# Performance work log

Hardware: AMD Instinct MI355X
Metric: run time of the kernel (lower is better)

## Reference

```python
import jax, jax.numpy as jnp
import numpy as np

D_MODEL, D_K, D_V = 1024, 64, 64
B, S = 4, 4096

def setup_inputs() -> dict:
    key = jax.random.key(0)
    ks = jax.random.split(key, 9)
    s_in = 1.0 / np.sqrt(D_MODEL)
    return {
        "Q": jax.random.normal(ks[0], (B, S, D_MODEL), jnp.float32),
        "K": jax.random.normal(ks[1], (B, S, D_MODEL), jnp.float32),
        "V": jax.random.normal(ks[2], (B, S, D_MODEL), jnp.float32),
        "Wq": jax.random.uniform(ks[3], (D_MODEL, D_K), jnp.float32, -s_in, s_in),
        "bq": jax.random.uniform(ks[4], (D_K,), jnp.float32, -s_in, s_in),
        "Wk": jax.random.uniform(ks[5], (D_MODEL, D_K), jnp.float32, -s_in, s_in),
        "bk": jax.random.uniform(ks[6], (D_K,), jnp.float32, -s_in, s_in),
        "Wv": jax.random.uniform(ks[7], (D_MODEL, D_V), jnp.float32, -s_in, s_in),
        "bv": jax.random.uniform(ks[8], (D_V,), jnp.float32, -s_in, s_in),
    }

def reference(Q, K, V, Wq, bq, Wk, bk, Wv, bv):
    # Linear projections: [B,S,d_model] -> [B,S,d_k/d_v]
    q = jnp.einsum("bsm,mk->bsk", Q, Wq) + bq
    k = jnp.einsum("btm,mk->btk", K, Wk) + bk
    v = jnp.einsum("btm,mv->btv", V, Wv) + bv
    # Scaled dot-product attention, softmax over key axis (dim=2)
    scores = jnp.einsum("bsk,btk->bst", q, k) / jnp.sqrt(jnp.float32(D_K))
    attn = jax.nn.softmax(scores, axis=2)  # [B,S,S]
    return jnp.einsum("bst,btv->bsv", attn, v)
```

## Files before the change

kernel.cpp:

```cpp
#include <hip/hip_runtime.h>

typedef __bf16 bf16;
typedef __attribute__((ext_vector_type(8))) __bf16 bf16x8;
typedef __attribute__((ext_vector_type(4))) float f32x4;
typedef __attribute__((ext_vector_type(16))) float f32x16;

#define MFMA16(a, b, c) __builtin_amdgcn_mfma_f32_16x16x32_bf16((a), (b), (c), 0, 0, 0)
#define MFMA32(a, b, c) __builtin_amdgcn_mfma_f32_32x32x16_bf16((a), (b), (c), 0, 0, 0)

typedef __attribute__((address_space(3))) unsigned int lds_u32_t;
typedef __attribute__((address_space(1))) unsigned int glb_u32_t;

__device__ __forceinline__ void gl2lds16(const void* g, void* l) {
    __builtin_amdgcn_global_load_lds((const glb_u32_t*)g, (lds_u32_t*)l, 16, 0, 0);
}

__device__ __forceinline__ bf16 tobf(float f) {
    unsigned u = __float_as_uint(f);
    u += 0x7fffu + ((u >> 16) & 1u);
    unsigned short h = (unsigned short)(u >> 16);
    bf16 r;
    __builtin_memcpy(&r, &h, 2);
    return r;
}

__device__ __forceinline__ bf16x8 cvt8h(f32x4 a, f32x4 b) {
    bf16x8 r;
    r[0] = (bf16)a[0]; r[1] = (bf16)a[1]; r[2] = (bf16)a[2]; r[3] = (bf16)a[3];
    r[4] = (bf16)b[0]; r[5] = (bf16)b[1]; r[6] = (bf16)b[2]; r[7] = (bf16)b[3];
    return r;
}

__global__ void wconv_kernel(const float* __restrict__ Wq, const float* __restrict__ Wk,
                             const float* __restrict__ Wv, bf16* __restrict__ Wt) {
    int j = blockIdx.y;
    const float* W = (j == 0) ? Wq : ((j == 1) ? Wk : Wv);
    int idx = blockIdx.x * 256 + threadIdx.x;
    int m = idx >> 6, n = idx & 63;
    Wt[(size_t)j * 65536 + (size_t)n * 1024 + m] = tobf(W[idx]);
}

__launch_bounds__(256, 3)
__global__ void proj_kernel(const float* __restrict__ Q, const float* __restrict__ K,
                            const float* __restrict__ V, const bf16* __restrict__ Wt,
                            const float* __restrict__ bq, const float* __restrict__ bk,
                            const float* __restrict__ bv,
                            bf16* __restrict__ q_ws, bf16* __restrict__ k_ws,
                            bf16* __restrict__ vT_ws) {
    const int j = blockIdx.y;
    const float* In   = (j == 0) ? Q : ((j == 1) ? K : V);
    const float* bias = (j == 0) ? bq : ((j == 1) ? bk : bv);
    const bf16* W = Wt + (size_t)j * 65536;

    __shared__ char smem[49152];
    char* As = smem;
    char* Bs = smem + 32768;

    const int tid = threadIdx.x;
    const int wave = tid >> 6, lane = tid & 63;
    const int quad = lane >> 4, l16 = lane & 15;
    const int rbase_blk = blockIdx.x * 64;

    f32x4 acc[4];
#pragma unroll
    for (int nt = 0; nt < 4; nt++) acc[nt] = {0.f, 0.f, 0.f, 0.f};

    for (int kc = 0; kc < 1024; kc += 128) {
#pragma unroll
        for (int i = 0; i < 8; i++) {
            int u = i * 256 + tid;
            int row = u >> 5, cg = u & 31;
            int cgg = cg ^ (row & 31);
            const float* g = In + (size_t)(rbase_blk + row) * 1024 + kc + cgg * 4;
            gl2lds16(g, As + (size_t)(i * 256 + wave * 64) * 16);
        }
#pragma unroll
        for (int i = 0; i < 4; i++) {
            int u = i * 256 + tid;
            int n = u >> 4, cg = u & 15;
            int cgg = cg ^ (n & 15);
            const bf16* g = W + (size_t)n * 1024 + kc + cgg * 8;
            gl2lds16(g, Bs + (size_t)(i * 256 + wave * 64) * 16);
        }
        __syncthreads();

        const int r = wave * 16 + l16;
#pragma unroll
        for (int p = 0; p < 4; p++) {
            int cg0 = (p * 8 + quad * 2) ^ (r & 31);
            int cg1 = (p * 8 + quad * 2 + 1) ^ (r & 31);
            f32x4 a0 = *(const f32x4*)(As + (size_t)r * 512 + cg0 * 16);
            f32x4 a1 = *(const f32x4*)(As + (size_t)r * 512 + cg1 * 16);
            bf16x8 av = cvt8h(a0, a1);
#pragma unroll
            for (int nt = 0; nt < 4; nt++) {
                int n = nt * 16 + l16;
                int cgb = (p * 4 + quad) ^ (n & 15);
                bf16x8 bv = *(const bf16x8*)(Bs + (size_t)n * 256 + cgb * 16);
                acc[nt] = MFMA16(av, bv, acc[nt]);
            }
        }
        __syncthreads();
    }

    const float scale = (j == 0) ? 0.125f * 1.44269504088896f : 1.0f;

    if (j != 2) {
        bf16* dst = (j == 0) ? q_ws : k_ws;
#pragma unroll
        for (int nt = 0; nt < 4; nt++) {
            int n = nt * 16 + l16;
            float bb = bias[n];
#pragma unroll
            for (int r4 = 0; r4 < 4; r4++) {
                int row = rbase_blk + wave * 16 + quad * 4 + r4;
                dst[(size_t)row * 64 + n] = tobf((acc[nt][r4] + bb) * scale);
            }
        }
    } else {
        bf16 (*vtile)[72] = (bf16(*)[72])smem;
#pragma unroll
        for (int nt = 0; nt < 4; nt++) {
            int n = nt * 16 + l16;
            float bb = bias[n];
#pragma unroll
            for (int r4 = 0; r4 < 4; r4++) {
                vtile[n][wave * 16 + quad * 4 + r4] = tobf(acc[nt][r4] + bb);
            }
        }
        __syncthreads();
        int gb = rbase_blk;
        int bi = gb >> 12, t0 = gb & 4095;
        int d = tid >> 2, part = (tid & 3) * 16;
        bf16x8 x0 = *(const bf16x8*)&vtile[d][part];
        bf16x8 x1 = *(const bf16x8*)&vtile[d][part + 8];
        bf16* dst = vT_ws + (size_t)(bi * 64 + d) * 4096 + t0 + part;
        *(bf16x8*)dst = x0;
        *(bf16x8*)(dst + 8) = x1;
    }
}

__launch_bounds__(256, 4)
__global__ void attn_kernel(const bf16* __restrict__ q_ws, const bf16* __restrict__ k_ws,
                            const bf16* __restrict__ vT_ws,
                            float* __restrict__ po, float* __restrict__ pl,
                            float* __restrict__ out, int keys_per_split, int direct) {
    const int b = blockIdx.z, split = blockIdx.y;
    const int tid = threadIdx.x, wave = tid >> 6, lane = tid & 63;
    const int l32 = lane & 31, h = lane >> 5;

    __shared__ bf16 kt[64][72];
    __shared__ bf16 vt[64][72];
    __shared__ bf16 pt[4][32][72];

    const int qrow0 = b * 4096 + blockIdx.x * 128 + wave * 32;

    bf16x8 qf[4];
    const bf16* qp = q_ws + (size_t)(qrow0 + l32) * 64 + h * 8;
#pragma unroll
    for (int c = 0; c < 4; c++) qf[c] = *(const bf16x8*)(qp + c * 16);

    f32x16 o0, o1;
    float l[16];
#pragma unroll
    for (int i = 0; i < 16; i++) { o0[i] = 0.f; o1[i] = 0.f; l[i] = 0.f; }

    const int key0 = split * keys_per_split;
    const int srow = tid >> 3, scol = (tid & 7) * 8;
    const bf16* kg = k_ws + (size_t)(b * 4096 + key0 + srow) * 64 + scol;
    const bf16* vg = vT_ws + (size_t)(b * 64 + srow) * 4096 + key0 + scol;

    uint4 kv0 = *(const uint4*)kg;
    uint4 kv1 = *(const uint4*)(kg + 2048);
    uint4 vv0 = *(const uint4*)vg;
    uint4 vv1 = *(const uint4*)(vg + 131072);

    for (int t0 = 0; t0 < keys_per_split; t0 += 64) {
        __syncthreads();
        *(uint4*)&kt[srow][scol]      = kv0;
        *(uint4*)&kt[srow + 32][scol] = kv1;
        *(uint4*)&vt[srow][scol]      = vv0;
        *(uint4*)&vt[srow + 32][scol] = vv1;
        if (t0 + 64 < keys_per_split) {
            kv0 = *(const uint4*)(kg + (size_t)(t0 + 64) * 64);
            kv1 = *(const uint4*)(kg + (size_t)(t0 + 64) * 64 + 2048);
            vv0 = *(const uint4*)(vg + t0 + 64);
            vv1 = *(const uint4*)(vg + t0 + 64 + 131072);
        }
        __syncthreads();

#pragma unroll
        for (int kt32 = 0; kt32 < 2; kt32++) {
            f32x16 s;
#pragma unroll
            for (int i = 0; i < 16; i++) s[i] = 0.f;
#pragma unroll
            for (int c = 0; c < 4; c++) {
                bf16x8 kf = *(const bf16x8*)(&kt[kt32 * 32 + l32][c * 16 + h * 8]);
                s = MFMA32(qf[c], kf, s);
            }
#pragma unroll
            for (int i = 0; i < 16; i++) {
                float p = __builtin_amdgcn_exp2f(s[i]);
                l[i] += p;
                int R = (i & 3) + 8 * (i >> 2) + 4 * h;
                pt[wave][R][kt32 * 32 + l32] = (bf16)p;
            }
        }

#pragma unroll
        for (int tc = 0; tc < 4; tc++) {
            bf16x8 pf  = *(const bf16x8*)(&pt[wave][l32][tc * 16 + h * 8]);
            bf16x8 vf0 = *(const bf16x8*)(&vt[l32][tc * 16 + h * 8]);
            bf16x8 vf1 = *(const bf16x8*)(&vt[32 + l32][tc * 16 + h * 8]);
            o0 = MFMA32(pf, vf0, o0);
            o1 = MFMA32(pf, vf1, o1);
        }
    }

#pragma unroll
    for (int i = 0; i < 16; i++) {
        float v = l[i];
        v += __shfl_xor(v, 1);  v += __shfl_xor(v, 2);  v += __shfl_xor(v, 4);
        v += __shfl_xor(v, 8);  v += __shfl_xor(v, 16);
        l[i] = v;
    }

    if (direct) {
        float* orow = out + (size_t)qrow0 * 64;
#pragma unroll
        for (int i = 0; i < 16; i++) {
            int R = (i & 3) + 8 * (i >> 2) + 4 * h;
            float inv = 1.0f / l[i];
            orow[(size_t)R * 64 + l32]      = o0[i] * inv;
            orow[(size_t)R * 64 + 32 + l32] = o1[i] * inv;
        }
    } else {
        size_t prow = (size_t)split * 16384 + qrow0;
        float* pob = po + prow * 64;
#pragma unroll
        for (int i = 0; i < 16; i++) {
            int R = (i & 3) + 8 * (i >> 2) + 4 * h;
            pob[(size_t)R * 64 + l32]      = o0[i];
            pob[(size_t)R * 64 + 32 + l32] = o1[i];
            if (l32 == 0) pl[prow + R] = l[i];
        }
    }
}

__launch_bounds__(256)
__global__ void combine_kernel(const float* __restrict__ po, const float* __restrict__ pl,
                               float* __restrict__ out, int nsplit) {
    int idx = blockIdx.x * 256 + threadIdx.x;
    int row = idx >> 6;
    float so = 0.f, sl = 0.f;
    for (int s = 0; s < nsplit; s++) {
        so += po[(size_t)s * 1048576 + idx];
        sl += pl[(size_t)s * 16384 + row];
    }
    out[idx] = so / sl;
}

extern "C" void kernel_launch(void* const* d_in, const int* in_sizes, int n_in,
                              void* d_out, int out_size, void* d_ws, size_t ws_size,
                              hipStream_t stream) {
    const float* Q  = (const float*)d_in[0];
    const float* K  = (const float*)d_in[1];
    const float* V  = (const float*)d_in[2];
    const float* Wq = (const float*)d_in[3];
    const float* bq = (const float*)d_in[4];
    const float* Wk = (const float*)d_in[5];
    const float* bk = (const float*)d_in[6];
    const float* Wv = (const float*)d_in[7];
    const float* bv = (const float*)d_in[8];
    float* out = (float*)d_out;

    char* ws = (char*)d_ws;
    bf16* Wt    = (bf16*)ws;
    bf16* q_ws  = (bf16*)(ws + 393216);
    bf16* k_ws  = (bf16*)(ws + 393216 + 2097152);
    bf16* vT_ws = (bf16*)(ws + 393216 + 2 * 2097152);
    const size_t base = 393216 + 3 * 2097152;

    const size_t per_split = 16384u * 4u + 1048576u * 4u;
    int nsplit = 1;
    if (ws_size >= base + 8 * per_split) nsplit = 8;
    else if (ws_size >= base + 4 * per_split) nsplit = 4;
    else if (ws_size >= base + 2 * per_split) nsplit = 2;

    float* pl = (float*)(ws + base);
    float* po = (float*)(ws + base + (size_t)nsplit * 65536);

    hipLaunchKernelGGL(wconv_kernel, dim3(256, 3), dim3(256), 0, stream, Wq, Wk, Wv, Wt);
    hipLaunchKernelGGL(proj_kernel, dim3(256, 3), dim3(256), 0, stream,
                       Q, K, V, Wt, bq, bk, bv, q_ws, k_ws, vT_ws);
    hipLaunchKernelGGL(attn_kernel, dim3(32, nsplit, 4), dim3(256), 0, stream,
                       q_ws, k_ws, vT_ws, po, pl, out, 4096 / nsplit, nsplit == 1 ? 1 : 0);
    if (nsplit > 1) {
        hipLaunchKernelGGL(combine_kernel, dim3(4096), dim3(256), 0, stream, po, pl, out, nsplit);
    }
}
```

Measured before the change: 260.3 us.

## Swap QK operand order, XOR-swizzle attention LDS tiles, shrink projection blocks

The attention kernel now computes S transposed, with K as the A operand, so each lane holds one query row's scores. This turns the per-row sum into one lane-local accumulator plus a single shuffle, replacing sixteen five-step reductions, and lets P be written to LDS as packed 4-element stores. The K, V and P LDS tiles drop their padding and use an XOR swizzle to avoid bank conflicts. The projection kernel moves to 128-thread blocks covering 32 rows with 64-wide K chunks and smaller LDS, doubling the grid. The row-sum lookup at the end now needs per-row shuffles, and the smaller projection tiles reuse weights less.

```diff
diff --git a/kernel.cpp b/kernel.cpp
--- a/kernel.cpp
+++ b/kernel.cpp
@@ -1,6 +1,7 @@
 #include <hip/hip_runtime.h>
 
 typedef __bf16 bf16;
+typedef __attribute__((ext_vector_type(4))) __bf16 bf16x4;
 typedef __attribute__((ext_vector_type(8))) __bf16 bf16x8;
 typedef __attribute__((ext_vector_type(4))) float f32x4;
 typedef __attribute__((ext_vector_type(16))) float f32x16;
@@ -40,7 +41,7 @@
     Wt[(size_t)j * 65536 + (size_t)n * 1024 + m] = tobf(W[idx]);
 }
 
-__launch_bounds__(256, 3)
+__launch_bounds__(128, 3)
 __global__ void proj_kernel(const float* __restrict__ Q, const float* __restrict__ K,
                             const float* __restrict__ V, const bf16* __restrict__ Wt,
                             const float* __restrict__ bq, const float* __restrict__ bk,
@@ -52,51 +53,51 @@
     const float* bias = (j == 0) ? bq : ((j == 1) ? bk : bv);
     const bf16* W = Wt + (size_t)j * 65536;
 
-    __shared__ char smem[49152];
+    __shared__ char smem[16384];
     char* As = smem;
-    char* Bs = smem + 32768;
+    char* Bs = smem + 8192;
 
     const int tid = threadIdx.x;
     const int wave = tid >> 6, lane = tid & 63;
     const int quad = lane >> 4, l16 = lane & 15;
-    const int rbase_blk = blockIdx.x * 64;
+    const int rbase = blockIdx.x * 32;
 
     f32x4 acc[4];
 #pragma unroll
     for (int nt = 0; nt < 4; nt++) acc[nt] = {0.f, 0.f, 0.f, 0.f};
 
-    for (int kc = 0; kc < 1024; kc += 128) {
-#pragma unroll
-        for (int i = 0; i < 8; i++) {
-            int u = i * 256 + tid;
-            int row = u >> 5, cg = u & 31;
-            int cgg = cg ^ (row & 31);
-            const float* g = In + (size_t)(rbase_blk + row) * 1024 + kc + cgg * 4;
-            gl2lds16(g, As + (size_t)(i * 256 + wave * 64) * 16);
-        }
+    for (int kc = 0; kc < 1024; kc += 64) {
 #pragma unroll
         for (int i = 0; i < 4; i++) {
-            int u = i * 256 + tid;
-            int n = u >> 4, cg = u & 15;
-            int cgg = cg ^ (n & 15);
-            const bf16* g = W + (size_t)n * 1024 + kc + cgg * 8;
-            gl2lds16(g, Bs + (size_t)(i * 256 + wave * 64) * 16);
+            int u = i * 128 + tid;
+            int row = u >> 4, cg = u & 15;
+            int cgg = cg ^ (row & 15);
+            gl2lds16(In + (size_t)(rbase + row) * 1024 + kc + cgg * 4,
+                     As + (size_t)(i * 128 + wave * 64) * 16);
+        }
+#pragma unroll
+        for (int i = 0; i < 4; i++) {
+            int u = i * 128 + tid;
+            int n = u >> 3, cg = u & 7;
+            int cgg = cg ^ (n & 7);
+            gl2lds16(W + (size_t)n * 1024 + kc + cgg * 8,
+                     Bs + (size_t)(i * 128 + wave * 64) * 16);
         }
         __syncthreads();
 
         const int r = wave * 16 + l16;
 #pragma unroll
-        for (int p = 0; p < 4; p++) {
-            int cg0 = (p * 8 + quad * 2) ^ (r & 31);
-            int cg1 = (p * 8 + quad * 2 + 1) ^ (r & 31);
-            f32x4 a0 = *(const f32x4*)(As + (size_t)r * 512 + cg0 * 16);
-            f32x4 a1 = *(const f32x4*)(As + (size_t)r * 512 + cg1 * 16);
+        for (int p = 0; p < 2; p++) {
+            int cg0 = (p * 8 + quad * 2) ^ (r & 15);
+            int cg1 = (p * 8 + quad * 2 + 1) ^ (r & 15);
+            f32x4 a0 = *(const f32x4*)(As + (size_t)r * 256 + cg0 * 16);
+            f32x4 a1 = *(const f32x4*)(As + (size_t)r * 256 + cg1 * 16);
             bf16x8 av = cvt8h(a0, a1);
 #pragma unroll
             for (int nt = 0; nt < 4; nt++) {
                 int n = nt * 16 + l16;
-                int cgb = (p * 4 + quad) ^ (n & 15);
-                bf16x8 bv = *(const bf16x8*)(Bs + (size_t)n * 256 + cgb * 16);
+                int cgb = (p * 4 + quad) ^ (n & 7);
+                bf16x8 bv = *(const bf16x8*)(Bs + (size_t)n * 128 + cgb * 16);
                 acc[nt] = MFMA16(av, bv, acc[nt]);
             }
         }
@@ -113,12 +114,12 @@
             float bb = bias[n];
 #pragma unroll
             for (int r4 = 0; r4 < 4; r4++) {
-                int row = rbase_blk + wave * 16 + quad * 4 + r4;
+                int row = rbase + wave * 16 + quad * 4 + r4;
                 dst[(size_t)row * 64 + n] = tobf((acc[nt][r4] + bb) * scale);
             }
         }
     } else {
-        bf16 (*vtile)[72] = (bf16(*)[72])smem;
+        bf16 (*vtile)[40] = (bf16(*)[40])smem;
 #pragma unroll
         for (int nt = 0; nt < 4; nt++) {
             int n = nt * 16 + l16;
@@ -129,12 +130,11 @@
             }
         }
         __syncthreads();
-        int gb = rbase_blk;
-        int bi = gb >> 12, t0 = gb & 4095;
-        int d = tid >> 2, part = (tid & 3) * 16;
-        bf16x8 x0 = *(const bf16x8*)&vtile[d][part];
-        bf16x8 x1 = *(const bf16x8*)&vtile[d][part + 8];
-        bf16* dst = vT_ws + (size_t)(bi * 64 + d) * 4096 + t0 + part;
+        int bi = rbase >> 12, t0 = rbase & 4095;
+        int d = tid & 63, sel = tid >> 6;
+        bf16x8 x0 = *(const bf16x8*)&vtile[d][sel * 16];
+        bf16x8 x1 = *(const bf16x8*)&vtile[d][sel * 16 + 8];
+        bf16* dst = vT_ws + (size_t)(bi * 64 + d) * 4096 + t0 + sel * 16;
         *(bf16x8*)dst = x0;
         *(bf16x8*)(dst + 8) = x1;
     }
@@ -148,10 +148,11 @@
     const int b = blockIdx.z, split = blockIdx.y;
     const int tid = threadIdx.x, wave = tid >> 6, lane = tid & 63;
     const int l32 = lane & 31, h = lane >> 5;
-
-    __shared__ bf16 kt[64][72];
-    __shared__ bf16 vt[64][72];
-    __shared__ bf16 pt[4][32][72];
+    const int sw = l32 & 7;
+
+    __shared__ bf16 kt[64][64];
+    __shared__ bf16 vt[64][64];
+    __shared__ bf16 pt[4][32][64];
 
     const int qrow0 = b * 4096 + blockIdx.x * 128 + wave * 32;
 
@@ -161,14 +162,16 @@
     for (int c = 0; c < 4; c++) qf[c] = *(const bf16x8*)(qp + c * 16);
 
     f32x16 o0, o1;
-    float l[16];
-#pragma unroll
-    for (int i = 0; i < 16; i++) { o0[i] = 0.f; o1[i] = 0.f; l[i] = 0.f; }
+    float l_lane = 0.f;
+#pragma unroll
+    for (int i = 0; i < 16; i++) { o0[i] = 0.f; o1[i] = 0.f; }
 
     const int key0 = split * keys_per_split;
-    const int srow = tid >> 3, scol = (tid & 7) * 8;
-    const bf16* kg = k_ws + (size_t)(b * 4096 + key0 + srow) * 64 + scol;
-    const bf16* vg = vT_ws + (size_t)(b * 64 + srow) * 4096 + key0 + scol;
+    const int srow = tid >> 3;
+    const int sg = tid & 7;
+    const int sgk = sg ^ (srow & 7);
+    const bf16* kg = k_ws + (size_t)(b * 4096 + key0 + srow) * 64 + sg * 8;
+    const bf16* vg = vT_ws + (size_t)(b * 64 + srow) * 4096 + key0 + sg * 8;
 
     uint4 kv0 = *(const uint4*)kg;
     uint4 kv1 = *(const uint4*)(kg + 2048);
@@ -177,10 +180,10 @@
 
     for (int t0 = 0; t0 < keys_per_split; t0 += 64) {
         __syncthreads();
-        *(uint4*)&kt[srow][scol]      = kv0;
-        *(uint4*)&kt[srow + 32][scol] = kv1;
-        *(uint4*)&vt[srow][scol]      = vv0;
-        *(uint4*)&vt[srow + 32][scol] = vv1;
+        *(uint4*)&kt[srow][sgk * 8]      = kv0;
+        *(uint4*)&kt[srow + 32][sgk * 8] = kv1;
+        *(uint4*)&vt[srow][sgk * 8]      = vv0;
+        *(uint4*)&vt[srow + 32][sgk * 8] = vv1;
         if (t0 + 64 < keys_per_split) {
             kv0 = *(const uint4*)(kg + (size_t)(t0 + 64) * 64);
             kv1 = *(const uint4*)(kg + (size_t)(t0 + 64) * 64 + 2048);
@@ -196,42 +199,42 @@
             for (int i = 0; i < 16; i++) s[i] = 0.f;
 #pragma unroll
             for (int c = 0; c < 4; c++) {
-                bf16x8 kf = *(const bf16x8*)(&kt[kt32 * 32 + l32][c * 16 + h * 8]);
-                s = MFMA32(qf[c], kf, s);
-            }
-#pragma unroll
-            for (int i = 0; i < 16; i++) {
-                float p = __builtin_amdgcn_exp2f(s[i]);
-                l[i] += p;
-                int R = (i & 3) + 8 * (i >> 2) + 4 * h;
-                pt[wave][R][kt32 * 32 + l32] = (bf16)p;
+                bf16x8 kf = *(const bf16x8*)(&kt[kt32 * 32 + l32][((2 * c + h) ^ sw) * 8]);
+                s = MFMA32(kf, qf[c], s);
+            }
+#pragma unroll
+            for (int g = 0; g < 4; g++) {
+                float p0 = __builtin_amdgcn_exp2f(s[4 * g + 0]);
+                float p1 = __builtin_amdgcn_exp2f(s[4 * g + 1]);
+                float p2 = __builtin_amdgcn_exp2f(s[4 * g + 2]);
+                float p3 = __builtin_amdgcn_exp2f(s[4 * g + 3]);
+                l_lane += (p0 + p1) + (p2 + p3);
+                bf16x4 pk;
+                pk[0] = (bf16)p0; pk[1] = (bf16)p1; pk[2] = (bf16)p2; pk[3] = (bf16)p3;
+                int gp = (kt32 * 4 + g) ^ sw;
+                *(bf16x4*)(&pt[wave][l32][gp * 8 + 4 * h]) = pk;
             }
         }
 
 #pragma unroll
         for (int tc = 0; tc < 4; tc++) {
-            bf16x8 pf  = *(const bf16x8*)(&pt[wave][l32][tc * 16 + h * 8]);
-            bf16x8 vf0 = *(const bf16x8*)(&vt[l32][tc * 16 + h * 8]);
-            bf16x8 vf1 = *(const bf16x8*)(&vt[32 + l32][tc * 16 + h * 8]);
+            int gp = ((2 * tc + h) ^ sw) * 8;
+            bf16x8 pf  = *(const bf16x8*)(&pt[wave][l32][gp]);
+            bf16x8 vf0 = *(const bf16x8*)(&vt[l32][gp]);
+            bf16x8 vf1 = *(const bf16x8*)(&vt[32 + l32][gp]);
             o0 = MFMA32(pf, vf0, o0);
             o1 = MFMA32(pf, vf1, o1);
         }
     }
 
-#pragma unroll
-    for (int i = 0; i < 16; i++) {
-        float v = l[i];
-        v += __shfl_xor(v, 1);  v += __shfl_xor(v, 2);  v += __shfl_xor(v, 4);
-        v += __shfl_xor(v, 8);  v += __shfl_xor(v, 16);
-        l[i] = v;
-    }
+    l_lane += __shfl_xor(l_lane, 32);
 
     if (direct) {
         float* orow = out + (size_t)qrow0 * 64;
 #pragma unroll
         for (int i = 0; i < 16; i++) {
             int R = (i & 3) + 8 * (i >> 2) + 4 * h;
-            float inv = 1.0f / l[i];
+            float inv = 1.0f / __shfl(l_lane, R);
             orow[(size_t)R * 64 + l32]      = o0[i] * inv;
             orow[(size_t)R * 64 + 32 + l32] = o1[i] * inv;
         }
@@ -243,8 +246,8 @@
             int R = (i & 3) + 8 * (i >> 2) + 4 * h;
             pob[(size_t)R * 64 + l32]      = o0[i];
             pob[(size_t)R * 64 + 32 + l32] = o1[i];
-            if (l32 == 0) pl[prow + R] = l[i];
-        }
+        }
+        if (h == 0) pl[prow + l32] = l_lane;
     }
 }
 
@@ -292,7 +295,7 @@
     float* po = (float*)(ws + base + (size_t)nsplit * 65536);
 
     hipLaunchKernelGGL(wconv_kernel, dim3(256, 3), dim3(256), 0, stream, Wq, Wk, Wv, Wt);
-    hipLaunchKernelGGL(proj_kernel, dim3(256, 3), dim3(256), 0, stream,
+    hipLaunchKernelGGL(proj_kernel, dim3(512, 3), dim3(128), 0, stream,
                        Q, K, V, Wt, bq, bk, bv, q_ws, k_ws, vT_ws);
     hipLaunchKernelGGL(attn_kernel, dim3(32, nsplit, 4), dim3(256), 0, stream,
                        q_ws, k_ws, vT_ws, po, pl, out, 4096 / nsplit, nsplit == 1 ? 1 : 0);
```

Result: faster. 252.2 us (-3.1%).
